# Optimization experiments

Measured on AMD Instinct MI355X. Metric: run time of the kernel, lower is better.

## Reference

```python
import jax, jax.numpy as jnp
import numpy as np

N_NODES = 50000
N_EDGES = 800000
IN_F, HID_F, OUT_F = 512, 128, 16


def setup_inputs() -> dict:
    key = jax.random.key(0)
    k1, k2, k3, k4, k5, k6 = jax.random.split(key, 6)
    x = jax.random.normal(k1, (N_NODES, IN_F), dtype=jnp.float32)
    edge_src = jax.random.randint(k2, (N_EDGES,), 0, N_NODES, dtype=jnp.int32)
    edge_dst = jax.random.randint(k3, (N_EDGES,), 0, N_NODES, dtype=jnp.int32)
    edge_val = jax.random.uniform(k4, (N_EDGES,), dtype=jnp.float32)
    # Xavier uniform init like torch.nn.init.xavier_uniform_
    lim1 = float(np.sqrt(6.0 / (IN_F + HID_F)))
    lim2 = float(np.sqrt(6.0 / (HID_F + OUT_F)))
    W1 = jax.random.uniform(k5, (IN_F, HID_F), minval=-lim1, maxval=lim1, dtype=jnp.float32)
    W2 = jax.random.uniform(k6, (HID_F, OUT_F), minval=-lim2, maxval=lim2, dtype=jnp.float32)
    return {"x": x, "edge_src": edge_src, "edge_dst": edge_dst, "edge_val": edge_val, "W1": W1, "W2": W2}


def _spmm(edge_val, edge_src, edge_dst, dense, n_nodes):
    # out[i] = sum_{e: dst(e)=i} val(e) * dense[src(e)]  == sparse_adj @ dense
    gathered = edge_val[:, None] * dense[edge_src]  # [E, F]
    return jax.ops.segment_sum(gathered, edge_dst, num_segments=n_nodes)


def reference(x, edge_src, edge_dst, edge_val, W1, W2):
    n = x.shape[0]
    # layer 1: mm -> spmm -> relu
    h = jax.nn.relu(_spmm(edge_val, edge_src, edge_dst, x @ W1, n))
    # dropout(p=0.5) is identity in eval mode (training=False)
    # layer 2: mm -> spmm (no relu)
    logits = _spmm(edge_val, edge_src, edge_dst, h @ W2, n)
    return jax.nn.log_softmax(logits, axis=1)
```

## Files before the change

kernel.cpp:

```cpp
#include <hip/hip_runtime.h>
#include <hip/hip_fp16.h>

#define N_NODES 50000
#define N_EDGES 800000
#define IN_F    512
#define HID_F   128
#define OUT_F   16
#define CAP     64
#define FAT_BLOCKS 782

typedef __attribute__((ext_vector_type(8))) short short8v;
typedef __attribute__((ext_vector_type(4))) float float4v;
typedef unsigned int uint32;
typedef unsigned short ushort16;

typedef __attribute__((address_space(3))) void lds_vp;
typedef __attribute__((address_space(1))) const void g_vp;

__device__ __forceinline__ ushort16 f2bf(float f) {
    uint32 u = __float_as_uint(f);
    uint32 r = (u + 0x7FFFu + ((u >> 16) & 1u)) >> 16;
    return (ushort16)r;
}
__device__ __forceinline__ float bf_lo(uint32 h) { return __uint_as_float(h << 16); }
__device__ __forceinline__ float bf_hi(uint32 h) { return __uint_as_float(h & 0xFFFF0000u); }
__device__ __forceinline__ float pk_val(uint32 u) {
    return __half2float(__ushort_as_half((unsigned short)(u >> 16)));
}

__global__ __launch_bounds__(256) void prep(const float* __restrict__ W1,
                                            unsigned short* __restrict__ W1T,
                                            int* __restrict__ cursor) {
    const int idx = blockIdx.x * 256 + threadIdx.x;
    if (idx < IN_F * HID_F) {
        const int k = idx >> 7;
        const int c = idx & 127;
        W1T[(size_t)c * IN_F + k] = (unsigned short)f2bf(W1[idx]);
    }
    if (idx < N_NODES) cursor[idx] = 0;
}

__global__ __launch_bounds__(320) void fat_coop(
        const int* __restrict__ src, const int* __restrict__ dst,
        const float* __restrict__ val, int* __restrict__ cursor,
        uint32* __restrict__ bucket,
        const float* __restrict__ X, const short* __restrict__ W1T,
        ushort16* __restrict__ H0) {
    __shared__ float4  Xs[1024];
    __shared__ short8v Ws[1024];
    const int t = threadIdx.x;

    if (t >= 256) {
        const int lane = t - 256;
        const int base = blockIdx.x * 1024 + lane;
        int  dd[16], ss[16];
        float vv[16];
        bool ok[16];
#pragma unroll
        for (int q = 0; q < 16; ++q) {
            const int e  = base + q * 64;
            ok[q] = (e < N_EDGES);
            const int ec = ok[q] ? e : 0;
            dd[q] = dst[ec]; ss[q] = src[ec]; vv[q] = val[ec];
        }
#pragma unroll
        for (int q = 0; q < 16; ++q) {
            if (ok[q]) {
                const int p = atomicAdd(&cursor[dd[q]], 1);
                if (p < CAP) {
                    const unsigned short hb = __half_as_ushort(__float2half_rn(vv[q]));
                    bucket[(size_t)dd[q] * CAP + p] = (uint32)ss[q] | ((uint32)hb << 16);
                }
            }
            __syncthreads();
        }
        return;
    }

    const int lane = t & 63;
    const int w    = t >> 6;
    const int l15  = lane & 15;
    const int kg   = (lane >> 4) * 8;
    const int bm   = blockIdx.x * 64;

    float4v acc[8];
#pragma unroll
    for (int n = 0; n < 8; ++n) acc[n] = (float4v){0.f, 0.f, 0.f, 0.f};

    const int ra = w * 16 + l15;

    for (int k0 = 0; k0 < IN_F; k0 += 64) {
#pragma unroll
        for (int i = 0; i < 4; ++i) {
            const int idx = i * 256 + t;
            const int r   = idx >> 4;
            const int s   = idx & 15;
            const int c4  = s ^ (r & 15);
            const int grow = min(bm + r, N_NODES - 1);
            const float* g = X + (size_t)grow * IN_F + k0 + c4 * 4;
            __builtin_amdgcn_global_load_lds((g_vp*)g, (lds_vp*)&Xs[idx], 16, 0, 0);
        }
#pragma unroll
        for (int i = 0; i < 4; ++i) {
            const int idx = i * 256 + t;
            const int col = idx >> 3;
            const int s   = idx & 7;
            const int gsl = s ^ (col & 7);
            const short* g = W1T + (size_t)col * IN_F + k0 + gsl * 8;
            __builtin_amdgcn_global_load_lds((g_vp*)g, (lds_vp*)&Ws[idx], 16, 0, 0);
        }
        __syncthreads();
#pragma unroll
        for (int ks = 0; ks < 64; ks += 32) {
            const int j0 = (ks + kg) >> 2;
            const float4 a0 = Xs[ra * 16 + ((j0)     ^ (ra & 15))];
            const float4 a1 = Xs[ra * 16 + ((j0 + 1) ^ (ra & 15))];
            short8v af;
            af[0] = (short)f2bf(a0.x); af[1] = (short)f2bf(a0.y);
            af[2] = (short)f2bf(a0.z); af[3] = (short)f2bf(a0.w);
            af[4] = (short)f2bf(a1.x); af[5] = (short)f2bf(a1.y);
            af[6] = (short)f2bf(a1.z); af[7] = (short)f2bf(a1.w);
            const int gbn = (ks + kg) >> 3;
#pragma unroll
            for (int n = 0; n < 8; ++n) {
                const int col = n * 16 + l15;
                const short8v bf = Ws[col * 8 + (gbn ^ (col & 7))];
                acc[n] = __builtin_amdgcn_mfma_f32_16x16x32_bf16(af, bf, acc[n], 0, 0, 0);
            }
        }
        __syncthreads();
    }

    const int crow0 = bm + w * 16 + (lane >> 4) * 4;
#pragma unroll
    for (int rr = 0; rr < 4; ++rr) {
        const int grow = crow0 + rr;
        if (grow < N_NODES) {
#pragma unroll
            for (int n = 0; n < 8; ++n)
                H0[(size_t)grow * HID_F + n * 16 + l15] = f2bf(acc[n][rr]);
        }
    }
}

__global__ __launch_bounds__(256) void spmm1_g2(const uint32* __restrict__ H0u,
                                                const int* __restrict__ cursor,
                                                const uint32* __restrict__ bucket,
                                                const float* __restrict__ W2,
                                                float* __restrict__ H2) {
    __shared__ float w2s[HID_F * 17];
    __shared__ float s1[4][HID_F];
    const int t = threadIdx.x;
#pragma unroll
    for (int i = 0; i < 8; ++i) {
        const int idx = t + i * 256;
        w2s[(idx >> 4) * 17 + (idx & 15)] = W2[idx];
    }
    __syncthreads();

    const int wv   = t >> 6;
    const int r    = blockIdx.x * 4 + wv;
    const int lane = t & 63;
    const int cnt  = min(cursor[r], CAP);
    const uint32 pk = bucket[(size_t)r * CAP + lane];
    float a0 = 0.f, a1 = 0.f;
    int j = 0;
    for (; j + 16 <= cnt; j += 16) {
        uint32 uu[16], hh[16];
#pragma unroll
        for (int q = 0; q < 16; ++q) {
            uu[q] = __shfl(pk, j + q);
            hh[q] = H0u[(size_t)(uu[q] & 0xFFFF) * 64 + lane];
        }
#pragma unroll
        for (int q = 0; q < 16; ++q) {
            const float v = pk_val(uu[q]);
            a0 += v * bf_lo(hh[q]);
            a1 += v * bf_hi(hh[q]);
        }
    }
    for (; j + 8 <= cnt; j += 8) {
        uint32 uu[8], hh[8];
#pragma unroll
        for (int q = 0; q < 8; ++q) {
            uu[q] = __shfl(pk, j + q);
            hh[q] = H0u[(size_t)(uu[q] & 0xFFFF) * 64 + lane];
        }
#pragma unroll
        for (int q = 0; q < 8; ++q) {
            const float v = pk_val(uu[q]);
            a0 += v * bf_lo(hh[q]);
            a1 += v * bf_hi(hh[q]);
        }
    }
    for (; j < cnt; ++j) {
        const uint32 u = __shfl(pk, j);
        const uint32 h = H0u[(size_t)(u & 0xFFFF) * 64 + lane];
        const float v  = pk_val(u);
        a0 += v * bf_lo(h);
        a1 += v * bf_hi(h);
    }
    s1[wv][2 * lane]     = fmaxf(a0, 0.f);
    s1[wv][2 * lane + 1] = fmaxf(a1, 0.f);
    __syncthreads();

    const int g = lane >> 4;
    const int c = lane & 15;
    float acc = 0.f;
#pragma unroll
    for (int i = 0; i < 32; ++i) {
        const int k = 32 * g + ((i + 8 * g) & 31);
        acc += s1[wv][k] * w2s[k * 17 + c];
    }
    acc += __shfl_xor(acc, 16);
    acc += __shfl_xor(acc, 32);
    if (lane < 16) H2[(size_t)r * OUT_F + lane] = acc;
}

__global__ __launch_bounds__(256) void spmm2_ls(const float* __restrict__ H2,
                                                const int* __restrict__ cursor,
                                                const uint32* __restrict__ bucket,
                                                float* __restrict__ out) {
    const int r = blockIdx.x * 16 + (threadIdx.x >> 4);
    const int f = threadIdx.x & 15;
    if (r >= N_NODES) return;
    const int cnt = min(cursor[r], CAP);
    float acc = 0.f;
    for (int base = 0; base < cnt; base += 16) {
        const uint32 pk = bucket[(size_t)r * CAP + base + f];
        const int lim = min(16, cnt - base);
        int j = 0;
        for (; j + 8 <= lim; j += 8) {
            uint32 uu[8];
            float  hh[8];
#pragma unroll
            for (int q = 0; q < 8; ++q) {
                uu[q] = __shfl(pk, j + q, 16);
                hh[q] = H2[(size_t)(uu[q] & 0xFFFF) * OUT_F + f];
            }
#pragma unroll
            for (int q = 0; q < 8; ++q) acc += pk_val(uu[q]) * hh[q];
        }
        for (; j < lim; ++j) {
            const uint32 u = __shfl(pk, j, 16);
            acc += pk_val(u) * H2[(size_t)(u & 0xFFFF) * OUT_F + f];
        }
    }
    float m = acc;
#pragma unroll
    for (int off = 1; off < 16; off <<= 1) m = fmaxf(m, __shfl_xor(m, off, 16));
    const float ex = __expf(acc - m);
    float ss = ex;
#pragma unroll
    for (int off = 1; off < 16; off <<= 1) ss += __shfl_xor(ss, off, 16);
    out[(size_t)r * OUT_F + f] = acc - m - logf(ss);
}

extern "C" void kernel_launch(void* const* d_in, const int* in_sizes, int n_in,
                              void* d_out, int out_size, void* d_ws, size_t ws_size,
                              hipStream_t stream) {
    const float* x        = (const float*)d_in[0];
    const int*   edge_src = (const int*)d_in[1];
    const int*   edge_dst = (const int*)d_in[2];
    const float* edge_val = (const float*)d_in[3];
    const float* W1       = (const float*)d_in[4];
    const float* W2       = (const float*)d_in[5];
    float* out = (float*)d_out;

    char* ws = (char*)d_ws;
    size_t off = 0;
    ushort16* H0  = (ushort16*)(ws + off); off += (size_t)N_NODES * HID_F * 2;
    float* H2     = (float*)   (ws + off); off += (size_t)N_NODES * OUT_F * 4;
    uint32* bucket= (uint32*)  (ws + off); off += (size_t)N_NODES * CAP * 4;
    int*   cursor = (int*)     (ws + off); off += (size_t)N_NODES * 4;
    unsigned short* W1T = (unsigned short*)(ws + off); off += (size_t)IN_F * HID_F * 2;

    prep<<<(IN_F * HID_F + 255) / 256, 256, 0, stream>>>(W1, W1T, cursor);

    fat_coop<<<FAT_BLOCKS, 320, 0, stream>>>(edge_src, edge_dst, edge_val,
                                             cursor, bucket,
                                             x, (const short*)W1T, H0);

    spmm1_g2<<<N_NODES / 4, 256, 0, stream>>>((const uint32*)H0, cursor, bucket, W2, H2);

    spmm2_ls<<<(N_NODES + 15) / 16, 256, 0, stream>>>(H2, cursor, bucket, out);
}
```

Before: 119.2 us.

## Split fused bucket-fill/GEMM kernel and partition bucket fill by XCD destination range

Replaces the cooperative kernel, where one extra wavefront per block built the CSR-like edge buckets alongside the X@W1 GEMM, with two separate launches. The new fill kernel assigns each block to one of 8 destination-node ranges based on blockIdx mod 8. This appears to target the 8 XCDs so that the atomics and bucket writes for a range stay in one XCD's L2. The cost is that every edge's dst is read 8 times and the fill no longer overlaps with the GEMM, which adds a launch.

```diff
diff --git a/kernel.cpp b/kernel.cpp
--- a/kernel.cpp
+++ b/kernel.cpp
@@ -7,7 +7,11 @@
 #define HID_F   128
 #define OUT_F   16
 #define CAP     64
-#define FAT_BLOCKS 782
+#define NXCD    8
+#define RANGE   6250
+#define FILL_SCAN 2048
+#define FILL_GRP  391
+#define FILL_BLOCKS (FILL_GRP * NXCD)
 
 typedef __attribute__((ext_vector_type(8))) short short8v;
 typedef __attribute__((ext_vector_type(4))) float float4v;
@@ -40,43 +44,45 @@
     if (idx < N_NODES) cursor[idx] = 0;
 }
 
-__global__ __launch_bounds__(320) void fat_coop(
-        const int* __restrict__ src, const int* __restrict__ dst,
-        const float* __restrict__ val, int* __restrict__ cursor,
-        uint32* __restrict__ bucket,
-        const float* __restrict__ X, const short* __restrict__ W1T,
-        ushort16* __restrict__ H0) {
+__global__ __launch_bounds__(256) void fill_v3(const int* __restrict__ src,
+                                               const int* __restrict__ dst,
+                                               const float* __restrict__ val,
+                                               int* __restrict__ cursor,
+                                               uint32* __restrict__ bucket) {
+    const int g   = blockIdx.x & 7;
+    const int blk = blockIdx.x >> 3;
+    const int lo  = g * RANGE;
+    const int hi  = lo + RANGE;
+    const int e0  = blk * FILL_SCAN + threadIdx.x;
+    int dd[8]; bool ok[8];
+#pragma unroll
+    for (int q = 0; q < 8; ++q) {
+        const int e  = e0 + q * 256;
+        const int ec = min(e, N_EDGES - 1);
+        dd[q] = dst[ec];
+        ok[q] = (e < N_EDGES) && (dd[q] >= lo) && (dd[q] < hi);
+    }
+#pragma unroll
+    for (int q = 0; q < 8; ++q) {
+        if (ok[q]) {
+            const int e = e0 + q * 256;
+            const int s = src[e];
+            const float v = val[e];
+            const int p = atomicAdd(&cursor[dd[q]], 1);
+            if (p < CAP) {
+                const unsigned short hb = __half_as_ushort(__float2half_rn(v));
+                bucket[(size_t)dd[q] * CAP + p] = (uint32)s | ((uint32)hb << 16);
+            }
+        }
+    }
+}
+
+__global__ __launch_bounds__(256) void gemm1_lds(const float* __restrict__ X,
+                                                 const short* __restrict__ W1T,
+                                                 ushort16* __restrict__ H0) {
     __shared__ float4  Xs[1024];
     __shared__ short8v Ws[1024];
-    const int t = threadIdx.x;
-
-    if (t >= 256) {
-        const int lane = t - 256;
-        const int base = blockIdx.x * 1024 + lane;
-        int  dd[16], ss[16];
-        float vv[16];
-        bool ok[16];
-#pragma unroll
-        for (int q = 0; q < 16; ++q) {
-            const int e  = base + q * 64;
-            ok[q] = (e < N_EDGES);
-            const int ec = ok[q] ? e : 0;
-            dd[q] = dst[ec]; ss[q] = src[ec]; vv[q] = val[ec];
-        }
-#pragma unroll
-        for (int q = 0; q < 16; ++q) {
-            if (ok[q]) {
-                const int p = atomicAdd(&cursor[dd[q]], 1);
-                if (p < CAP) {
-                    const unsigned short hb = __half_as_ushort(__float2half_rn(vv[q]));
-                    bucket[(size_t)dd[q] * CAP + p] = (uint32)ss[q] | ((uint32)hb << 16);
-                }
-            }
-            __syncthreads();
-        }
-        return;
-    }
-
+    const int t    = threadIdx.x;
     const int lane = t & 63;
     const int w    = t >> 6;
     const int l15  = lane & 15;
@@ -277,9 +283,9 @@
 
     prep<<<(IN_F * HID_F + 255) / 256, 256, 0, stream>>>(W1, W1T, cursor);
 
-    fat_coop<<<FAT_BLOCKS, 320, 0, stream>>>(edge_src, edge_dst, edge_val,
-                                             cursor, bucket,
-                                             x, (const short*)W1T, H0);
+    fill_v3<<<FILL_BLOCKS, 256, 0, stream>>>(edge_src, edge_dst, edge_val, cursor, bucket);
+
+    gemm1_lds<<<(N_NODES + 63) / 64, 256, 0, stream>>>(x, (const short*)W1T, H0);
 
     spmm1_g2<<<N_NODES / 4, 256, 0, stream>>>((const uint32*)H0, cursor, bucket, W2, H2);
 
```

After: 132.4 us. 11.1% more time.
